# Kernel optimization log

Measured on AMD Instinct MI355X. Metric: run time of the kernel, lower is better.

The kernel has to match this reference:

```python
import jax, jax.numpy as jnp
import numpy as np

R = 32  # low-rank dim hard-coded in HyperNetwork


def setup_inputs() -> dict:
    key = jax.random.key(0)
    ks = jax.random.split(key, 7)
    B, L, H = 16, 8192, 8
    Ts, Dh = 64, 256
    target_ipt = jax.random.normal(ks[0], (B, L, Ts), dtype=jnp.float32)
    hyper_ipt = jax.random.normal(ks[1], (H, Dh), dtype=jnp.float32)
    hyp_mask = jax.random.uniform(ks[2], (B, L, H, 1), dtype=jnp.float32)
    # hypernet params; scale down so generated weights are O(1)
    W1 = jax.random.normal(ks[3], (Dh, 2 * Ts * R), dtype=jnp.float32) * 0.02
    b1 = jax.random.normal(ks[4], (2 * Ts * R,), dtype=jnp.float32) * 0.02
    Wb = jax.random.normal(ks[5], (Dh, Ts), dtype=jnp.float32) * 0.02
    bb = jax.random.normal(ks[6], (Ts,), dtype=jnp.float32) * 0.02
    return {"target_ipt": target_ipt, "hyper_ipt": hyper_ipt, "hyp_mask": hyp_mask,
            "W1": W1, "b1": b1, "Wb": Wb, "bb": bb}


def reference(target_ipt, hyper_ipt, hyp_mask, W1, b1, Wb, bb):
    Ts = Wb.shape[1]
    H = hyper_ipt.shape[0]
    # HyperNetwork: generate per-condition low-rank weight factors and bias
    hw = hyper_ipt @ W1 + b1                     # (H, 2*Ts*R)
    down = hw[:, : Ts * R].reshape(H, Ts, R)     # (H, Ts, R)
    up = hw[:, Ts * R:].reshape(H, R, Ts)        # (H, R, Ts)
    bias = hyper_ipt @ Wb + bb                   # (H, Ts)
    # Materialize full per-condition weight, as the original does (down @ up)
    W = jnp.einsum('htr,hrs->hts', down, up)     # (H, Ts, Ts)
    # target_linear: (B,L,1,1,Ts) @ (H,Ts,Ts) -> squeeze -> (B,L,H,Ts), + bias
    lin = jnp.einsum('bld,hds->blhs', target_ipt, W) + bias[None, None]
    # masked sum over hyper-batch dim H
    return (lin * hyp_mask).sum(axis=-2)         # (B, L, Ts)
```

## Files before the change

### kernel.cpp

```cpp
#include <hip/hip_runtime.h>
#include <hip/hip_bf16.h>

typedef __attribute__((ext_vector_type(8))) short bf16x8;
typedef __attribute__((ext_vector_type(4))) float f32x4;

static __device__ __forceinline__ unsigned short f2bf(float f) {
    unsigned int u = __float_as_uint(f);
    unsigned int rnd = 0x7FFFu + ((u >> 16) & 1u);
    return (unsigned short)((u + rnd) >> 16);
}

static __device__ __forceinline__ bf16x8 cvt8(float4 u, float4 v) {
    union { bf16x8 r; __hip_bfloat162 h[4]; } o;
    o.h[0] = __float22bfloat162_rn(float2{u.x, u.y});
    o.h[1] = __float22bfloat162_rn(float2{u.z, u.w});
    o.h[2] = __float22bfloat162_rn(float2{v.x, v.y});
    o.h[3] = __float22bfloat162_rn(float2{v.z, v.w});
    return o.r;
}

__global__ __launch_bounds__(256)
void hypernet_kernel(const float* __restrict__ hyper,
                     const float* __restrict__ W1,
                     const float* __restrict__ b1,
                     const float* __restrict__ Wb,
                     const float* __restrict__ bb,
                     float* __restrict__ hw,
                     float* __restrict__ bias)
{
    __shared__ float red[256];
    const int tid = threadIdx.x;
    const int p   = tid >> 5;
    const int jj  = tid & 31;
    const int o0  = blockIdx.x * 32;
    const int o   = o0 + jj;

    float acc = 0.f;
    if (o0 < 8 * 4096) {
        int h = o >> 12, j = o & 4095;
        const float* hr = hyper + (h << 8);
        #pragma unroll
        for (int i = 0; i < 32; ++i) {
            int d = (p << 5) + i;
            acc += hr[d] * W1[d * 4096 + j];
        }
    } else {
        int t = o - 8 * 4096;
        int h = t >> 6, s = t & 63;
        const float* hr = hyper + (h << 8);
        #pragma unroll
        for (int i = 0; i < 32; ++i) {
            int d = (p << 5) + i;
            acc += hr[d] * Wb[d * 64 + s];
        }
    }
    red[tid] = acc;
    __syncthreads();
    if (p == 0) {
        float sum = red[jj]       + red[32 + jj]  + red[64 + jj]  + red[96 + jj]
                  + red[128 + jj] + red[160 + jj] + red[192 + jj] + red[224 + jj];
        if (o0 < 8 * 4096) hw[o] = sum + b1[o & 4095];
        else {
            int t = o - 8 * 4096;
            bias[t] = sum + bb[t & 63];
        }
    }
}

__global__ void pack_kernel(const float* __restrict__ hw,
                            unsigned short* __restrict__ packed)
{
    int p = blockIdx.x * blockDim.x + threadIdx.x;
    int b   = p & 7;
    int l   = (p >> 3) & 63;
    int kap = (p >> 9) & 1;
    int n   = p >> 10;
    int k   = kap * 32 + ((l >> 4) << 3) + b;
    int col = (n << 4) + (l & 15);
    int h = col >> 6, s = col & 63;
    const float* hwh = hw + h * 4096;
    float acc = 0.f;
    #pragma unroll
    for (int r = 0; r < 32; ++r)
        acc += hwh[k * 32 + r] * hwh[2048 + r * 64 + s];
    packed[p] = f2bf(acc);
}

#define TPW 4

__global__ __launch_bounds__(256, 3)
void main_kernel(const float* __restrict__ X,
                 const float* __restrict__ Mask,
                 const unsigned short* __restrict__ packedB,
                 const float* __restrict__ bias,
                 float* __restrict__ Out)
{
    __shared__ float sM[16 * TPW * 8];

    const int tid  = threadIdx.x;
    const int lane = tid & 63;
    const int w    = tid >> 6;
    const int c    = lane & 15;
    const int g    = lane >> 4;
    const int rowBase = blockIdx.x * (16 * TPW);
    const int s = (w << 4) + c;

    {
        const float2* Mv = (const float2*)(Mask + (long)rowBase * 8);
        ((float2*)sM)[tid] = Mv[tid];
    }

    bf16x8 Bf[8][2];
    #pragma unroll
    for (int h = 0; h < 8; ++h) {
        const unsigned short* pb = packedB + ((((h * 4 + w) * 2) * 64) + lane) * 8;
        Bf[h][0] = *(const bf16x8*)pb;
        Bf[h][1] = *(const bf16x8*)(pb + 512);
    }

    float biasr[8];
    #pragma unroll
    for (int h = 0; h < 8; ++h) biasr[h] = bias[h * 64 + s];

    const float* xrow = X + (long)(rowBase + c) * 64 + (g << 3);

    float4 px0 = *(const float4*)(xrow);
    float4 px1 = *(const float4*)(xrow + 4);
    float4 px2 = *(const float4*)(xrow + 32);
    float4 px3 = *(const float4*)(xrow + 36);

    __syncthreads();

    #pragma unroll 2
    for (int t = 0; t < TPW; ++t) {
        float4 cx0 = px0, cx1 = px1, cx2 = px2, cx3 = px3;

        if (t + 1 < TPW) {
            const float* xp = xrow + (t + 1) * 1024;
            px0 = *(const float4*)(xp);
            px1 = *(const float4*)(xp + 4);
            px2 = *(const float4*)(xp + 32);
            px3 = *(const float4*)(xp + 36);
        }

        bf16x8 a0 = cvt8(cx0, cx1);
        bf16x8 a1 = cvt8(cx2, cx3);

        f32x4 acc[8];
        #pragma unroll
        for (int h = 0; h < 8; ++h) acc[h] = (f32x4)(0.f);
        #pragma unroll
        for (int h = 0; h < 8; ++h) {
            acc[h] = __builtin_amdgcn_mfma_f32_16x16x32_bf16(a0, Bf[h][0], acc[h], 0, 0, 0);
            acc[h] = __builtin_amdgcn_mfma_f32_16x16x32_bf16(a1, Bf[h][1], acc[h], 0, 0, 0);
        }

        #pragma unroll
        for (int i = 0; i < 4; ++i) {
            const int r = t * 16 + (g << 2) + i;
            const float4 ml = *(const float4*)(&sM[r * 8]);
            const float4 mh = *(const float4*)(&sM[r * 8 + 4]);
            float o = ml.x * (acc[0][i] + biasr[0]);
            o = fmaf(ml.y, acc[1][i] + biasr[1], o);
            o = fmaf(ml.z, acc[2][i] + biasr[2], o);
            o = fmaf(ml.w, acc[3][i] + biasr[3], o);
            o = fmaf(mh.x, acc[4][i] + biasr[4], o);
            o = fmaf(mh.y, acc[5][i] + biasr[5], o);
            o = fmaf(mh.z, acc[6][i] + biasr[6], o);
            o = fmaf(mh.w, acc[7][i] + biasr[7], o);
            Out[(long)(rowBase + r) * 64 + s] = o;
        }
    }
}

extern "C" void kernel_launch(void* const* d_in, const int* in_sizes, int n_in,
                              void* d_out, int out_size, void* d_ws, size_t ws_size,
                              hipStream_t stream) {
    const float* target = (const float*)d_in[0];
    const float* hyper  = (const float*)d_in[1];
    const float* mask   = (const float*)d_in[2];
    const float* W1     = (const float*)d_in[3];
    const float* b1     = (const float*)d_in[4];
    const float* Wb     = (const float*)d_in[5];
    const float* bb     = (const float*)d_in[6];
    float* out = (float*)d_out;

    float* hw   = (float*)d_ws;
    float* bias = hw + 8 * 4096;
    unsigned short* packed = (unsigned short*)(bias + 512);

    const int M = in_sizes[0] / 64;

    hipLaunchKernelGGL(hypernet_kernel, dim3((8 * 4096 + 8 * 64) / 32), dim3(256),
                       0, stream, hyper, W1, b1, Wb, bb, hw, bias);
    hipLaunchKernelGGL(pack_kernel, dim3(32768 / 256), dim3(256), 0, stream, hw, packed);
    hipLaunchKernelGGL(main_kernel, dim3(M / (16 * TPW)), dim3(256), 0, stream,
                       target, mask, packed, bias, out);
}
```

Baseline: 36.79 us.

## Make main kernel persistent with double-buffered mask and cross-group prefetch

Turns the main kernel into a grid-stride persistent kernel with 768 blocks. Each block loads the B fragments and bias once and then loops over 64-row groups, prefetching the next group's mask and X rows while it computes the current one. The mask tile is double-buffered in LDS with a padded stride to reduce bank conflicts, and the bias is folded into the MFMA accumulator initial value. This amortises per-block setup and hides load latency, at the cost of a fixed grid size and an extra __syncthreads per group.

```diff
diff --git a/kernel.cpp b/kernel.cpp
--- a/kernel.cpp
+++ b/kernel.cpp
@@ -86,29 +86,24 @@
     packed[p] = f2bf(acc);
 }
 
-#define TPW 4
+#define MSTRIDE 12
 
 __global__ __launch_bounds__(256, 3)
 void main_kernel(const float* __restrict__ X,
                  const float* __restrict__ Mask,
                  const unsigned short* __restrict__ packedB,
                  const float* __restrict__ bias,
-                 float* __restrict__ Out)
+                 float* __restrict__ Out,
+                 int M)
 {
-    __shared__ float sM[16 * TPW * 8];
+    __shared__ float sM[2][64 * MSTRIDE];
 
     const int tid  = threadIdx.x;
     const int lane = tid & 63;
     const int w    = tid >> 6;
     const int c    = lane & 15;
     const int g    = lane >> 4;
-    const int rowBase = blockIdx.x * (16 * TPW);
-    const int s = (w << 4) + c;
-
-    {
-        const float2* Mv = (const float2*)(Mask + (long)rowBase * 8);
-        ((float2*)sM)[tid] = Mv[tid];
-    }
+    const int s    = (w << 4) + c;
 
     bf16x8 Bf[8][2];
     #pragma unroll
@@ -117,59 +112,76 @@
         Bf[h][0] = *(const bf16x8*)pb;
         Bf[h][1] = *(const bf16x8*)(pb + 512);
     }
-
     float biasr[8];
     #pragma unroll
     for (int h = 0; h < 8; ++h) biasr[h] = bias[h * 64 + s];
 
-    const float* xrow = X + (long)(rowBase + c) * 64 + (g << 3);
-
-    float4 px0 = *(const float4*)(xrow);
-    float4 px1 = *(const float4*)(xrow + 4);
-    float4 px2 = *(const float4*)(xrow + 32);
-    float4 px3 = *(const float4*)(xrow + 36);
-
-    __syncthreads();
-
-    #pragma unroll 2
-    for (int t = 0; t < TPW; ++t) {
-        float4 cx0 = px0, cx1 = px1, cx2 = px2, cx3 = px3;
-
-        if (t + 1 < TPW) {
-            const float* xp = xrow + (t + 1) * 1024;
-            px0 = *(const float4*)(xp);
-            px1 = *(const float4*)(xp + 4);
-            px2 = *(const float4*)(xp + 32);
-            px3 = *(const float4*)(xp + 36);
-        }
-
-        bf16x8 a0 = cvt8(cx0, cx1);
-        bf16x8 a1 = cvt8(cx2, cx3);
-
-        f32x4 acc[8];
+    const int NG = M >> 6;
+    const int stride = gridDim.x;
+
+    int gidx = blockIdx.x;
+    long rowBase = (long)gidx << 6;
+
+    float2 mreg = *(const float2*)(Mask + rowBase * 8 + tid * 2);
+    const float* xp0 = X + (rowBase + c) * 64 + (g << 3);
+    float4 px0 = *(const float4*)(xp0);
+    float4 px1 = *(const float4*)(xp0 + 4);
+    float4 px2 = *(const float4*)(xp0 + 32);
+    float4 px3 = *(const float4*)(xp0 + 36);
+
+    int buf = 0;
+    while (gidx < NG) {
+        *(float2*)(&sM[buf][(tid >> 2) * MSTRIDE + (tid & 3) * 2]) = mreg;
+        __syncthreads();
+
+        const int gnext = gidx + stride;
+        const long rowBaseNext = (gnext < NG) ? ((long)gnext << 6) : rowBase;
+
+        mreg = *(const float2*)(Mask + rowBaseNext * 8 + tid * 2);
+
         #pragma unroll
-        for (int h = 0; h < 8; ++h) acc[h] = (f32x4)(0.f);
-        #pragma unroll
-        for (int h = 0; h < 8; ++h) {
-            acc[h] = __builtin_amdgcn_mfma_f32_16x16x32_bf16(a0, Bf[h][0], acc[h], 0, 0, 0);
-            acc[h] = __builtin_amdgcn_mfma_f32_16x16x32_bf16(a1, Bf[h][1], acc[h], 0, 0, 0);
-        }
-
-        #pragma unroll
-        for (int i = 0; i < 4; ++i) {
-            const int r = t * 16 + (g << 2) + i;
-            const float4 ml = *(const float4*)(&sM[r * 8]);
-            const float4 mh = *(const float4*)(&sM[r * 8 + 4]);
-            float o = ml.x * (acc[0][i] + biasr[0]);
-            o = fmaf(ml.y, acc[1][i] + biasr[1], o);
-            o = fmaf(ml.z, acc[2][i] + biasr[2], o);
-            o = fmaf(ml.w, acc[3][i] + biasr[3], o);
-            o = fmaf(mh.x, acc[4][i] + biasr[4], o);
-            o = fmaf(mh.y, acc[5][i] + biasr[5], o);
-            o = fmaf(mh.z, acc[6][i] + biasr[6], o);
-            o = fmaf(mh.w, acc[7][i] + biasr[7], o);
-            Out[(long)(rowBase + r) * 64 + s] = o;
-        }
+        for (int t = 0; t < 4; ++t) {
+            float4 cx0 = px0, cx1 = px1, cx2 = px2, cx3 = px3;
+
+            const float* xq = (t < 3)
+                ? X + (rowBase + (t + 1) * 16 + c) * 64 + (g << 3)
+                : X + (rowBaseNext + c) * 64 + (g << 3);
+            px0 = *(const float4*)(xq);
+            px1 = *(const float4*)(xq + 4);
+            px2 = *(const float4*)(xq + 32);
+            px3 = *(const float4*)(xq + 36);
+
+            bf16x8 a0 = cvt8(cx0, cx1);
+            bf16x8 a1 = cvt8(cx2, cx3);
+
+            f32x4 acc[8];
+            #pragma unroll
+            for (int h = 0; h < 8; ++h) acc[h] = (f32x4)(biasr[h]);
+            #pragma unroll
+            for (int h = 0; h < 8; ++h) {
+                acc[h] = __builtin_amdgcn_mfma_f32_16x16x32_bf16(a0, Bf[h][0], acc[h], 0, 0, 0);
+                acc[h] = __builtin_amdgcn_mfma_f32_16x16x32_bf16(a1, Bf[h][1], acc[h], 0, 0, 0);
+            }
+
+            #pragma unroll
+            for (int i = 0; i < 4; ++i) {
+                const int r = t * 16 + (g << 2) + i;
+                const float4 ml = *(const float4*)(&sM[buf][r * MSTRIDE]);
+                const float4 mh = *(const float4*)(&sM[buf][r * MSTRIDE + 4]);
+                float o = ml.x * acc[0][i];
+                o = fmaf(ml.y, acc[1][i], o);
+                o = fmaf(ml.z, acc[2][i], o);
+                o = fmaf(ml.w, acc[3][i], o);
+                o = fmaf(mh.x, acc[4][i], o);
+                o = fmaf(mh.y, acc[5][i], o);
+                o = fmaf(mh.z, acc[6][i], o);
+                o = fmaf(mh.w, acc[7][i], o);
+                Out[(rowBase + r) * 64 + s] = o;
+            }
+        }
+        buf ^= 1;
+        gidx = gnext;
+        rowBase = rowBaseNext;
     }
 }
 
@@ -194,6 +206,6 @@
     hipLaunchKernelGGL(hypernet_kernel, dim3((8 * 4096 + 8 * 64) / 32), dim3(256),
                        0, stream, hyper, W1, b1, Wb, bb, hw, bias);
     hipLaunchKernelGGL(pack_kernel, dim3(32768 / 256), dim3(256), 0, stream, hw, packed);
-    hipLaunchKernelGGL(main_kernel, dim3(M / (16 * TPW)), dim3(256), 0, stream,
-                       target, mask, packed, bias, out);
-}
+    hipLaunchKernelGGL(main_kernel, dim3(768), dim3(256), 0, stream,
+                       target, mask, packed, bias, out, M);
+}
```

New measurement: 70.27 us. 1.91x slower.

## Make main kernel persistent with double-buffered swizzled LDS staging of X and mask

Applied to the files above, without the earlier changes.

The main kernel now runs as a fixed grid of 1024 blocks. Each block loops over 32-row groups and double-buffers X and mask tiles through shared memory: the next group's global loads are prefetched into registers while the current group's MFMAs run. X is stored with coalesced row-wise loads and an XOR swizzle to avoid bank conflicts, bias is folded into the accumulator init, and the 8 heads are split into two halves of 4 to cut register pressure so occupancy can rise to 4 blocks per SIMD. The trade-off is an LDS round trip and a barrier per group. It also assumes M divides evenly by 1024×32.

```diff
diff --git a/kernel.cpp b/kernel.cpp
--- a/kernel.cpp
+++ b/kernel.cpp
@@ -86,29 +86,39 @@
     packed[p] = f2bf(acc);
 }
 
-#define TPW 4
-
-__global__ __launch_bounds__(256, 3)
+#define GR 32
+
+__global__ __launch_bounds__(256, 4)
 void main_kernel(const float* __restrict__ X,
                  const float* __restrict__ Mask,
                  const unsigned short* __restrict__ packedB,
                  const float* __restrict__ bias,
-                 float* __restrict__ Out)
+                 float* __restrict__ Out,
+                 int M)
 {
-    __shared__ float sM[16 * TPW * 8];
+    __shared__ __align__(16) float sX[2][GR * 64];
+    __shared__ __align__(16) float sM[2][GR * 12];
 
     const int tid  = threadIdx.x;
     const int lane = tid & 63;
     const int w    = tid >> 6;
     const int c    = lane & 15;
     const int g    = lane >> 4;
-    const int rowBase = blockIdx.x * (16 * TPW);
-    const int s = (w << 4) + c;
-
-    {
-        const float2* Mv = (const float2*)(Mask + (long)rowBase * 8);
-        ((float2*)sM)[tid] = Mv[tid];
-    }
+    const int s    = (w << 4) + c;
+
+    const int rowsPerBlock = M / gridDim.x;
+    const int ngrp = rowsPerBlock / GR;
+    const int blockRow = blockIdx.x * rowsPerBlock;
+
+    const int srow = tid >> 3;
+    const int sw8  = (tid & 7) << 3;
+    const int xoff = srow * 64 + (sw8 ^ ((srow & 7) << 3));
+    const int sxw  = srow * 64 + sw8;
+    const int smw  = (tid >> 3) * 12 + (tid & 7);
+
+    float4 p0 = *(const float4*)(X + blockRow * 64 + xoff);
+    float4 p1 = *(const float4*)(X + blockRow * 64 + xoff + 4);
+    float  pm = Mask[blockRow * 8 + tid];
 
     bf16x8 Bf[8][2];
     #pragma unroll
@@ -117,59 +127,94 @@
         Bf[h][0] = *(const bf16x8*)pb;
         Bf[h][1] = *(const bf16x8*)(pb + 512);
     }
-
     float biasr[8];
     #pragma unroll
     for (int h = 0; h < 8; ++h) biasr[h] = bias[h * 64 + s];
 
-    const float* xrow = X + (long)(rowBase + c) * 64 + (g << 3);
-
-    float4 px0 = *(const float4*)(xrow);
-    float4 px1 = *(const float4*)(xrow + 4);
-    float4 px2 = *(const float4*)(xrow + 32);
-    float4 px3 = *(const float4*)(xrow + 36);
-
+    *(float4*)(&sX[0][sxw])     = p0;
+    *(float4*)(&sX[0][sxw + 4]) = p1;
+    sM[0][smw] = pm;
     __syncthreads();
 
-    #pragma unroll 2
-    for (int t = 0; t < TPW; ++t) {
-        float4 cx0 = px0, cx1 = px1, cx2 = px2, cx3 = px3;
-
-        if (t + 1 < TPW) {
-            const float* xp = xrow + (t + 1) * 1024;
-            px0 = *(const float4*)(xp);
-            px1 = *(const float4*)(xp + 4);
-            px2 = *(const float4*)(xp + 32);
-            px3 = *(const float4*)(xp + 36);
-        }
-
-        bf16x8 a0 = cvt8(cx0, cx1);
-        bf16x8 a1 = cvt8(cx2, cx3);
-
-        f32x4 acc[8];
+    int buf = 0;
+    for (int grp = 0; grp < ngrp; ++grp) {
+        const int gRow = blockRow + grp * GR;
+        const bool more = (grp + 1 < ngrp);
+
+        if (more) {
+            const float* xb = X + (gRow + GR) * 64;
+            p0 = *(const float4*)(xb + xoff);
+            p1 = *(const float4*)(xb + xoff + 4);
+            pm = Mask[(gRow + GR) * 8 + tid];
+        }
+
+        const float* sx = sX[buf];
+        const float* sm = sM[buf];
+        const int sz = (c & 7) << 3;
+
         #pragma unroll
-        for (int h = 0; h < 8; ++h) acc[h] = (f32x4)(0.f);
-        #pragma unroll
-        for (int h = 0; h < 8; ++h) {
-            acc[h] = __builtin_amdgcn_mfma_f32_16x16x32_bf16(a0, Bf[h][0], acc[h], 0, 0, 0);
-            acc[h] = __builtin_amdgcn_mfma_f32_16x16x32_bf16(a1, Bf[h][1], acc[h], 0, 0, 0);
-        }
-
-        #pragma unroll
-        for (int i = 0; i < 4; ++i) {
-            const int r = t * 16 + (g << 2) + i;
-            const float4 ml = *(const float4*)(&sM[r * 8]);
-            const float4 mh = *(const float4*)(&sM[r * 8 + 4]);
-            float o = ml.x * (acc[0][i] + biasr[0]);
-            o = fmaf(ml.y, acc[1][i] + biasr[1], o);
-            o = fmaf(ml.z, acc[2][i] + biasr[2], o);
-            o = fmaf(ml.w, acc[3][i] + biasr[3], o);
-            o = fmaf(mh.x, acc[4][i] + biasr[4], o);
-            o = fmaf(mh.y, acc[5][i] + biasr[5], o);
-            o = fmaf(mh.z, acc[6][i] + biasr[6], o);
-            o = fmaf(mh.w, acc[7][i] + biasr[7], o);
-            Out[(long)(rowBase + r) * 64 + s] = o;
-        }
+        for (int t = 0; t < 2; ++t) {
+            const int rb = ((t << 4) + c) * 64;
+            float4 x0 = *(const float4*)(&sx[rb + (((g << 3)     ) ^ sz)]);
+            float4 x1 = *(const float4*)(&sx[rb + (((g << 3)     ) ^ sz) + 4]);
+            float4 x2 = *(const float4*)(&sx[rb + (((g << 3) + 32) ^ sz)]);
+            float4 x3 = *(const float4*)(&sx[rb + (((g << 3) + 32) ^ sz) + 4]);
+
+            bf16x8 a0 = cvt8(x0, x1);
+            bf16x8 a1 = cvt8(x2, x3);
+
+            float o[4];
+            {
+                f32x4 acc[4];
+                #pragma unroll
+                for (int h = 0; h < 4; ++h) acc[h] = (f32x4)(biasr[h]);
+                #pragma unroll
+                for (int h = 0; h < 4; ++h) {
+                    acc[h] = __builtin_amdgcn_mfma_f32_16x16x32_bf16(a0, Bf[h][0], acc[h], 0, 0, 0);
+                    acc[h] = __builtin_amdgcn_mfma_f32_16x16x32_bf16(a1, Bf[h][1], acc[h], 0, 0, 0);
+                }
+                #pragma unroll
+                for (int i = 0; i < 4; ++i) {
+                    const int rr = (t << 4) + (g << 2) + i;
+                    const float4 ml = *(const float4*)(&sm[rr * 12]);
+                    float v = ml.x * acc[0][i];
+                    v = fmaf(ml.y, acc[1][i], v);
+                    v = fmaf(ml.z, acc[2][i], v);
+                    v = fmaf(ml.w, acc[3][i], v);
+                    o[i] = v;
+                }
+            }
+            {
+                f32x4 acc[4];
+                #pragma unroll
+                for (int h = 0; h < 4; ++h) acc[h] = (f32x4)(biasr[4 + h]);
+                #pragma unroll
+                for (int h = 0; h < 4; ++h) {
+                    acc[h] = __builtin_amdgcn_mfma_f32_16x16x32_bf16(a0, Bf[4 + h][0], acc[h], 0, 0, 0);
+                    acc[h] = __builtin_amdgcn_mfma_f32_16x16x32_bf16(a1, Bf[4 + h][1], acc[h], 0, 0, 0);
+                }
+                #pragma unroll
+                for (int i = 0; i < 4; ++i) {
+                    const int rr = (t << 4) + (g << 2) + i;
+                    const float4 mh = *(const float4*)(&sm[rr * 12 + 4]);
+                    float v = o[i];
+                    v = fmaf(mh.x, acc[0][i], v);
+                    v = fmaf(mh.y, acc[1][i], v);
+                    v = fmaf(mh.z, acc[2][i], v);
+                    v = fmaf(mh.w, acc[3][i], v);
+                    Out[(gRow + rr) * 64 + s] = v;
+                }
+            }
+        }
+
+        if (more) {
+            float* sxn = sX[buf ^ 1];
+            *(float4*)(&sxn[sxw])     = p0;
+            *(float4*)(&sxn[sxw + 4]) = p1;
+            sM[buf ^ 1][smw] = pm;
+        }
+        __syncthreads();
+        buf ^= 1;
     }
 }
 
@@ -194,6 +239,6 @@
     hipLaunchKernelGGL(hypernet_kernel, dim3((8 * 4096 + 8 * 64) / 32), dim3(256),
                        0, stream, hyper, W1, b1, Wb, bb, hw, bias);
     hipLaunchKernelGGL(pack_kernel, dim3(32768 / 256), dim3(256), 0, stream, hw, packed);
-    hipLaunchKernelGGL(main_kernel, dim3(M / (16 * TPW)), dim3(256), 0, stream,
-                       target, mask, packed, bias, out);
-}
+    hipLaunchKernelGGL(main_kernel, dim3(1024), dim3(256), 0, stream,
+                       target, mask, packed, bias, out, M);
+}
```

Measured after the change: 88.72 us. +141.1%, slower.
